# Kernel tuning notes

Measured on AMD Instinct MI355X. Metric: run time of the kernel, lower is better.

The kernel has to match this reference:

```python
import jax, jax.numpy as jnp
import numpy as np
from jax import lax


def setup_inputs() -> dict:
    key = jax.random.key(0)
    k1, k2 = jax.random.split(key)
    B, T, D, O = 8, 8192, 512, 512
    x = jax.random.normal(k1, (B, T, D), dtype=jnp.float32)
    # Dense kernel over concat([h_t, state]) -> width 2*D
    W = jax.random.normal(k2, (2 * D, O), dtype=jnp.float32) * (1.0 / np.sqrt(2 * D))
    b = jnp.zeros((O,), dtype=jnp.float32)
    decay = jnp.float32(0.95)
    return {"x": x, "W": W, "b": b, "decay": decay}


def reference(x, W, b, decay):
    # x: [B, T, D]; W: [2D, O]; b: [O]; decay: scalar lambda
    B, T, D = x.shape
    lam = jnp.clip(decay, 0.5, 0.999)  # keras constraint on the decay weight
    h_avg = jnp.mean(x, axis=0)  # [T, D] batch-mean per timestep

    # EMA recurrence: s_t = lam * s_{t-1} + (1 - lam) * h_avg_t, s_{-1} = 0
    def step(s, a):
        s = lam * s + (1.0 - lam) * a
        return s, s

    _, states = lax.scan(step, jnp.zeros((D,), x.dtype), h_avg)  # [T, D]

    # proj(concat([h_t, s_t])) = h_t @ W_h + s_t @ W_s + b (fused, no concat materialized)
    W_h, W_s = W[:D], W[D:]
    out = jnp.einsum('btd,do->bto', x, W_h) + jnp.einsum('td,do->to', states, W_s)[None] + b
    return out  # [B, T, O]
```

## Files before the change

kernel.cpp:

```cpp
#include <hip/hip_runtime.h>
#include <hip/hip_bf16.h>
#include <stdint.h>

#define T_DIM 8192
#define B_DIM 8
#define D_DIM 512
#define O_DIM 512

typedef __attribute__((ext_vector_type(4))) float f32x4;
typedef __attribute__((ext_vector_type(8))) short short8;
typedef __attribute__((ext_vector_type(4))) unsigned short us4;

__device__ __forceinline__ unsigned short f2bf(float f) {
  union { float f; uint32_t u; } v; v.f = f;
  uint32_t u = v.u + 0x7FFFu + ((v.u >> 16) & 1u);
  return (unsigned short)(u >> 16);
}

__device__ __forceinline__ uint32_t cvtpk(float a, float b) {
  uint32_t r;
  asm("v_cvt_pk_bf16_f32 %0, %1, %2" : "=v"(r) : "v"(a), "v"(b));
  return r;
}

__device__ __forceinline__ void gload_lds16(const void* g, void* l) {
  __builtin_amdgcn_global_load_lds(
      (const __attribute__((address_space(1))) void*)g,
      (__attribute__((address_space(3))) void*)l, 16, 0, 0);
}

__device__ __forceinline__ float clip_lam(const float* decay) {
  return fminf(fmaxf(decay[0], 0.5f), 0.999f);
}

__global__ void mean_kernel(const float* __restrict__ x, float* __restrict__ havg) {
  int idx = blockIdx.x * 256 + threadIdx.x;
  const f32x4* x4 = (const f32x4*)x;
  const size_t stride = (size_t)T_DIM * D_DIM / 4;
  f32x4 s = {0.f, 0.f, 0.f, 0.f};
#pragma unroll
  for (int b = 0; b < B_DIM; ++b) s += x4[(size_t)b * stride + idx];
  s *= 0.125f;
  ((f32x4*)havg)[idx] = s;
}

__global__ void wconv_kernel(const float* __restrict__ W, unsigned short* __restrict__ Wt) {
  __shared__ float tile[64][65];
  int bk = blockIdx.x >> 3;
  int bn = blockIdx.x & 7;
  int tr = threadIdx.x >> 4;
  int tc = threadIdx.x & 15;
#pragma unroll
  for (int i = 0; i < 4; ++i) {
    int row = i * 16 + tr;
    f32x4 v = *(const f32x4*)&W[(size_t)(bk * 64 + row) * O_DIM + bn * 64 + tc * 4];
#pragma unroll
    for (int j = 0; j < 4; ++j) tile[row][tc * 4 + j] = v[j];
  }
  __syncthreads();
#pragma unroll
  for (int i = 0; i < 4; ++i) {
    int nl = i * 16 + tr;
    us4 o;
#pragma unroll
    for (int j = 0; j < 4; ++j) o[j] = f2bf(tile[tc * 4 + j][nl]);
    int kg = bk * 64 + tc * 4;
    int h = kg >> 9;
    int k = kg & 511;
    *(us4*)&Wt[(size_t)h * (512 * 512) + (size_t)(bn * 64 + nl) * 512 + k] = o;
  }
}

#define CHUNK 128
#define NCHUNK (T_DIM / CHUNK)

__global__ void scanA_kernel(float* __restrict__ havg, const float* __restrict__ decay) {
  int chunk = blockIdx.x >> 1;
  int d = ((blockIdx.x & 1) << 8) + threadIdx.x;
  float lam = clip_lam(decay);
  float om = 1.0f - lam;
  size_t base = (size_t)chunk * CHUNK * D_DIM + d;
  float cur[16], nxt[16];
#pragma unroll
  for (int i = 0; i < 16; ++i) cur[i] = havg[base + (size_t)i * D_DIM];
  float s = 0.f;
  for (int blk = 0; blk < 8; ++blk) {
    if (blk < 7) {
#pragma unroll
      for (int i = 0; i < 16; ++i)
        nxt[i] = havg[base + (size_t)((blk + 1) * 16 + i) * D_DIM];
    }
#pragma unroll
    for (int i = 0; i < 16; ++i) {
      s = lam * s + om * cur[i];
      havg[base + (size_t)(blk * 16 + i) * D_DIM] = s;
    }
#pragma unroll
    for (int i = 0; i < 16; ++i) cur[i] = nxt[i];
  }
}

__global__ void scanB_kernel(const float* __restrict__ havg, const float* __restrict__ decay,
                             float* __restrict__ carry) {
  int d = blockIdx.x * 256 + threadIdx.x;
  float lam = clip_lam(decay);
  float l2 = lam * lam;
  float l4 = l2 * l2;
  float l8 = l4 * l4;
  float l16 = l8 * l8;
  float l32 = l16 * l16;
  float l64 = l32 * l32;
  float l128 = l64 * l64;
  float e[NCHUNK];
#pragma unroll
  for (int c = 0; c < NCHUNK; ++c)
    e[c] = havg[((size_t)c * CHUNK + CHUNK - 1) * D_DIM + d];
  float s = 0.f;
#pragma unroll
  for (int c = 0; c < NCHUNK; ++c) {
    s = l128 * s + e[c];
    carry[c * D_DIM + d] = s;
  }
}

__global__ void scanC_kernel(const float* __restrict__ havg, const float* __restrict__ carry,
                             const float* __restrict__ decay, unsigned short* __restrict__ st) {
  int idx = blockIdx.x * 256 + threadIdx.x;
  int t = idx >> 7;
  int d4 = idx & 127;
  int c = t >> 7;
  int k = t & 127;
  float lam = clip_lam(decay);
  float w = exp2f((float)(k + 1) * __log2f(lam));
  f32x4 p = ((const f32x4*)havg)[idx];
  f32x4 cin = {0.f, 0.f, 0.f, 0.f};
  if (c > 0) cin = ((const f32x4*)carry)[(size_t)(c - 1) * 128 + d4];
  us4 o;
#pragma unroll
  for (int j = 0; j < 4; ++j) o[j] = f2bf(p[j] + w * cin[j]);
  ((us4*)st)[idx] = o;
}

template <bool AF32, bool ADD_SBAR>
__global__ __launch_bounds__(256, 2)
void gemm128(const void* __restrict__ Av, const unsigned short* __restrict__ Bt,
             const float* __restrict__ extra, float* __restrict__ C) {
  constexpr int ABYTES = AF32 ? 16384 : 8192;
  __shared__ __align__(16) char smem[ABYTES + 8192];
  unsigned short* Bs = (unsigned short*)(smem + ABYTES);

  int nwg = gridDim.x;
  int bid = blockIdx.x;
  int swz = (bid & 7) * (nwg >> 3) + (bid >> 3);
  int tm = swz >> 2, tn = swz & 3;
  int brow = tm << 7, bcol = tn << 7;

  int tid = threadIdx.x;
  int wave = tid >> 6, lane = tid & 63;
  int wr = (wave >> 1) << 6, wc = (wave & 1) << 6;
  const int lr = lane & 15, lkb = lane >> 4;

  f32x4 acc[4][4];
#pragma unroll
  for (int m = 0; m < 4; ++m)
#pragma unroll
    for (int n = 0; n < 4; ++n) acc[m][n] = (f32x4){0.f, 0.f, 0.f, 0.f};

  for (int kt = 0; kt < 512 / 32; ++kt) {
    int k0 = kt << 5;
    if constexpr (AF32) {
      const float* Ag = (const float*)Av;
#pragma unroll
      for (int it = 0; it < 4; ++it) {
        int q = (it << 2) + wave;
        int row = (q << 3) + (lane >> 3);
        int kc = ((lane & 7) ^ (lane >> 3)) << 2;
        gload_lds16(Ag + (size_t)(brow + row) * 512 + k0 + kc, smem + (q << 10));
      }
    } else {
      const unsigned short* Ag = (const unsigned short*)Av;
#pragma unroll
      for (int it = 0; it < 2; ++it) {
        int q = (it << 2) + wave;
        int row = (q << 4) + (lane >> 2);
        int kc = (lane & 3) << 3;
        gload_lds16(Ag + (size_t)(brow + row) * 512 + k0 + kc, smem + (q << 10));
      }
    }
#pragma unroll
    for (int it = 0; it < 2; ++it) {
      int q = (it << 2) + wave;
      int n = (q << 4) + (lane >> 2);
      int kc = (lane & 3) << 3;
      gload_lds16(Bt + (size_t)(bcol + n) * 512 + k0 + kc, (char*)Bs + (q << 10));
    }
    __syncthreads();

    short8 af[4], bfr[4];
    if constexpr (AF32) {
      const float* As = (const float*)smem;
#pragma unroll
      for (int m = 0; m < 4; ++m) {
        int row = wr + (m << 4) + lr;
        int r7 = row & 7;
        int b0 = lkb << 1;
        f32x4 lo = *(const f32x4*)(As + row * 32 + ((b0 ^ r7) << 2));
        f32x4 hi = *(const f32x4*)(As + row * 32 + (((b0 + 1) ^ r7) << 2));
        union { short8 s; uint32_t u[4]; } t;
        t.u[0] = cvtpk(lo[0], lo[1]); t.u[1] = cvtpk(lo[2], lo[3]);
        t.u[2] = cvtpk(hi[0], hi[1]); t.u[3] = cvtpk(hi[2], hi[3]);
        af[m] = t.s;
      }
    } else {
      const unsigned short* As = (const unsigned short*)smem;
#pragma unroll
      for (int m = 0; m < 4; ++m)
        af[m] = *(const short8*)(As + (size_t)(wr + (m << 4) + lr) * 32 + (lkb << 3));
    }
#pragma unroll
    for (int n = 0; n < 4; ++n)
      bfr[n] = *(const short8*)(Bs + (size_t)(wc + (n << 4) + lr) * 32 + (lkb << 3));

#pragma unroll
    for (int m = 0; m < 4; ++m)
#pragma unroll
      for (int n = 0; n < 4; ++n)
        acc[m][n] = __builtin_amdgcn_mfma_f32_16x16x32_bf16(af[m], bfr[n], acc[m][n], 0, 0, 0);
    __syncthreads();
  }

#pragma unroll
  for (int m = 0; m < 4; ++m) {
    int row0 = brow + wr + (m << 4) + ((lane >> 4) << 2);
#pragma unroll
    for (int n = 0; n < 4; ++n) {
      int col = bcol + wc + (n << 4) + lr;
#pragma unroll
      for (int j = 0; j < 4; ++j) {
        int row = row0 + j;
        float v = acc[m][n][j];
        if constexpr (ADD_SBAR)
          v += extra[(size_t)(row & (T_DIM - 1)) * O_DIM + col];
        else
          v += extra[col];
        C[(size_t)row * O_DIM + col] = v;
      }
    }
  }
}

extern "C" void kernel_launch(void* const* d_in, const int* in_sizes, int n_in,
                              void* d_out, int out_size, void* d_ws, size_t ws_size,
                              hipStream_t stream) {
  (void)in_sizes; (void)n_in; (void)out_size; (void)ws_size;
  const float* x     = (const float*)d_in[0];
  const float* W     = (const float*)d_in[1];
  const float* bias  = (const float*)d_in[2];
  const float* decay = (const float*)d_in[3];
  float* out = (float*)d_out;

  char* ws = (char*)d_ws;
  float*          havg  = (float*)ws;
  unsigned short* st    = (unsigned short*)(ws + 16777216);
  unsigned short* Wt    = (unsigned short*)(ws + 16777216 + 8388608);
  float*          sbar  = (float*)(ws + 16777216 + 8388608 + 1048576);
  float*          carry = (float*)(ws + 16777216 + 8388608 + 1048576 + 16777216);

  mean_kernel<<<T_DIM * D_DIM / 4 / 256, 256, 0, stream>>>(x, havg);
  wconv_kernel<<<128, 256, 0, stream>>>(W, Wt);
  scanA_kernel<<<NCHUNK * 2, 256, 0, stream>>>(havg, decay);
  scanB_kernel<<<2, 256, 0, stream>>>(havg, decay, carry);
  scanC_kernel<<<T_DIM * D_DIM / 4 / 256, 256, 0, stream>>>(havg, carry, decay, st);
  gemm128<false, false><<<(T_DIM / 128) * 4, 256, 0, stream>>>(st, Wt + 512 * 512, bias, sbar);
  gemm128<true, true><<<(B_DIM * T_DIM / 128) * 4, 256, 0, stream>>>(x, Wt, sbar, out);
}
```

Measured before the change: 139.7 us.

## Double-buffer GEMM LDS tiles, swizzle bf16 LDS, vectorize epilogue via LDS

```diff
diff --git a/kernel.cpp b/kernel.cpp
--- a/kernel.cpp
+++ b/kernel.cpp
@@ -37,9 +37,10 @@
   int idx = blockIdx.x * 256 + threadIdx.x;
   const f32x4* x4 = (const f32x4*)x;
   const size_t stride = (size_t)T_DIM * D_DIM / 4;
-  f32x4 s = {0.f, 0.f, 0.f, 0.f};
-#pragma unroll
-  for (int b = 0; b < B_DIM; ++b) s += x4[(size_t)b * stride + idx];
+  f32x4 v[8];
+#pragma unroll
+  for (int b = 0; b < B_DIM; ++b) v[b] = x4[(size_t)b * stride + idx];
+  f32x4 s = ((v[0] + v[1]) + (v[2] + v[3])) + ((v[4] + v[5]) + (v[6] + v[7]));
   s *= 0.125f;
   ((f32x4*)havg)[idx] = s;
 }
@@ -142,12 +143,12 @@
 }
 
 template <bool AF32, bool ADD_SBAR>
-__global__ __launch_bounds__(256, 2)
+__global__ __launch_bounds__(256, AF32 ? 3 : 4)
 void gemm128(const void* __restrict__ Av, const unsigned short* __restrict__ Bt,
              const float* __restrict__ extra, float* __restrict__ C) {
   constexpr int ABYTES = AF32 ? 16384 : 8192;
-  __shared__ __align__(16) char smem[ABYTES + 8192];
-  unsigned short* Bs = (unsigned short*)(smem + ABYTES);
+  constexpr int BUFB = ABYTES + 8192;
+  __shared__ __align__(16) char smem[2][BUFB];
 
   int nwg = gridDim.x;
   int bid = blockIdx.x;
@@ -160,45 +161,63 @@
   int wr = (wave >> 1) << 6, wc = (wave & 1) << 6;
   const int lr = lane & 15, lkb = lane >> 4;
 
+  const int soct = ((lane & 3) ^ ((lane >> 3) & 3)) << 3;
+  const int pm = (lr >> 1) & 3;
+  const int kcA = ((lane & 7) ^ (lane >> 3)) << 2;
+
+  const size_t a_base = AF32
+      ? (size_t)(brow + (wave << 3) + (lane >> 3)) * 512 + kcA
+      : (size_t)(brow + (wave << 4) + (lane >> 2)) * 512 + soct;
+  const size_t b_base = (size_t)(bcol + (wave << 4) + (lane >> 2)) * 512 + soct;
+
   f32x4 acc[4][4];
 #pragma unroll
   for (int m = 0; m < 4; ++m)
 #pragma unroll
     for (int n = 0; n < 4; ++n) acc[m][n] = (f32x4){0.f, 0.f, 0.f, 0.f};
 
-  for (int kt = 0; kt < 512 / 32; ++kt) {
-    int k0 = kt << 5;
-    if constexpr (AF32) {
-      const float* Ag = (const float*)Av;
-#pragma unroll
-      for (int it = 0; it < 4; ++it) {
-        int q = (it << 2) + wave;
-        int row = (q << 3) + (lane >> 3);
-        int kc = ((lane & 7) ^ (lane >> 3)) << 2;
-        gload_lds16(Ag + (size_t)(brow + row) * 512 + k0 + kc, smem + (q << 10));
-      }
+#define STAGE(buf, kt_)                                                        \
+  {                                                                            \
+    int k0_ = (kt_) << 5;                                                      \
+    if constexpr (AF32) {                                                      \
+      const float* Ag = (const float*)Av;                                      \
+      _Pragma("unroll")                                                        \
+      for (int it = 0; it < 4; ++it)                                           \
+        gload_lds16(Ag + a_base + (size_t)(it << 14) + k0_,                    \
+                    &smem[buf][(((it << 2) + wave) << 10)]);                   \
+    } else {                                                                   \
+      const unsigned short* Ag = (const unsigned short*)Av;                    \
+      _Pragma("unroll")                                                        \
+      for (int it = 0; it < 2; ++it)                                           \
+        gload_lds16(Ag + a_base + (size_t)(it << 15) + k0_,                    \
+                    &smem[buf][(((it << 2) + wave) << 10)]);                   \
+    }                                                                          \
+    _Pragma("unroll")                                                          \
+    for (int it = 0; it < 2; ++it)                                             \
+      gload_lds16(Bt + b_base + (size_t)(it << 15) + k0_,                      \
+                  &smem[buf][ABYTES + (((it << 2) + wave) << 10)]);            \
+  }
+
+  STAGE(0, 0);
+
+#pragma unroll
+  for (int kt = 0; kt < 16; ++kt) {
+    const int cur = kt & 1;
+    if (kt < 15) {
+      STAGE(cur ^ 1, kt + 1);
+      if constexpr (AF32)
+        asm volatile("s_waitcnt vmcnt(6)" ::: "memory");
+      else
+        asm volatile("s_waitcnt vmcnt(4)" ::: "memory");
     } else {
-      const unsigned short* Ag = (const unsigned short*)Av;
-#pragma unroll
-      for (int it = 0; it < 2; ++it) {
-        int q = (it << 2) + wave;
-        int row = (q << 4) + (lane >> 2);
-        int kc = (lane & 3) << 3;
-        gload_lds16(Ag + (size_t)(brow + row) * 512 + k0 + kc, smem + (q << 10));
-      }
-    }
-#pragma unroll
-    for (int it = 0; it < 2; ++it) {
-      int q = (it << 2) + wave;
-      int n = (q << 4) + (lane >> 2);
-      int kc = (lane & 3) << 3;
-      gload_lds16(Bt + (size_t)(bcol + n) * 512 + k0 + kc, (char*)Bs + (q << 10));
-    }
-    __syncthreads();
+      asm volatile("s_waitcnt vmcnt(0)" ::: "memory");
+    }
+    __builtin_amdgcn_s_barrier();
+    __builtin_amdgcn_sched_barrier(0);
 
     short8 af[4], bfr[4];
     if constexpr (AF32) {
-      const float* As = (const float*)smem;
+      const float* As = (const float*)&smem[cur][0];
 #pragma unroll
       for (int m = 0; m < 4; ++m) {
         int row = wr + (m << 4) + lr;
@@ -212,40 +231,52 @@
         af[m] = t.s;
       }
     } else {
-      const unsigned short* As = (const unsigned short*)smem;
+      const unsigned short* As = (const unsigned short*)&smem[cur][0];
 #pragma unroll
       for (int m = 0; m < 4; ++m)
-        af[m] = *(const short8*)(As + (size_t)(wr + (m << 4) + lr) * 32 + (lkb << 3));
-    }
+        af[m] = *(const short8*)(As + (size_t)(wr + (m << 4) + lr) * 32 + ((lkb ^ pm) << 3));
+    }
+    const unsigned short* Bs = (const unsigned short*)&smem[cur][ABYTES];
 #pragma unroll
     for (int n = 0; n < 4; ++n)
-      bfr[n] = *(const short8*)(Bs + (size_t)(wc + (n << 4) + lr) * 32 + (lkb << 3));
+      bfr[n] = *(const short8*)(Bs + (size_t)(wc + (n << 4) + lr) * 32 + ((lkb ^ pm) << 3));
 
 #pragma unroll
     for (int m = 0; m < 4; ++m)
 #pragma unroll
       for (int n = 0; n < 4; ++n)
         acc[m][n] = __builtin_amdgcn_mfma_f32_16x16x32_bf16(af[m], bfr[n], acc[m][n], 0, 0, 0);
+
+    __builtin_amdgcn_sched_barrier(0);
+    __builtin_amdgcn_s_barrier();
+  }
+#undef STAGE
+
+  float* tp = (float*)&smem[0][0] + (size_t)wave * 2048;
+#pragma unroll
+  for (int m = 0; m < 4; ++m) {
+#pragma unroll
+    for (int n = 0; n < 4; ++n)
+#pragma unroll
+      for (int j = 0; j < 4; ++j)
+        tp[((lkb << 2) + j) * 68 + (n << 4) + lr] = acc[m][n][j];
     __syncthreads();
-  }
-
-#pragma unroll
-  for (int m = 0; m < 4; ++m) {
-    int row0 = brow + wr + (m << 4) + ((lane >> 4) << 2);
-#pragma unroll
-    for (int n = 0; n < 4; ++n) {
-      int col = bcol + wc + (n << 4) + lr;
-#pragma unroll
-      for (int j = 0; j < 4; ++j) {
-        int row = row0 + j;
-        float v = acc[m][n][j];
-        if constexpr (ADD_SBAR)
-          v += extra[(size_t)(row & (T_DIM - 1)) * O_DIM + col];
-        else
-          v += extra[col];
-        C[(size_t)row * O_DIM + col] = v;
-      }
-    }
+#pragma unroll
+    for (int p = 0; p < 4; ++p) {
+      int rl = (p << 2) + (lane >> 4);
+      int c0 = (lane & 15) << 2;
+      f32x4 v = *(const f32x4*)(tp + rl * 68 + c0);
+      int row = brow + wr + (m << 4) + rl;
+      int col = bcol + wc + c0;
+      f32x4 e;
+      if constexpr (ADD_SBAR)
+        e = *(const f32x4*)&extra[(size_t)(row & (T_DIM - 1)) * O_DIM + col];
+      else
+        e = *(const f32x4*)&extra[col];
+      v += e;
+      *(f32x4*)&C[(size_t)row * O_DIM + col] = v;
+    }
+    __syncthreads();
   }
 }
 
@@ -260,11 +291,12 @@
   float* out = (float*)d_out;
 
   char* ws = (char*)d_ws;
-  float*          havg  = (float*)ws;
-  unsigned short* st    = (unsigned short*)(ws + 16777216);
-  unsigned short* Wt    = (unsigned short*)(ws + 16777216 + 8388608);
-  float*          sbar  = (float*)(ws + 16777216 + 8388608 + 1048576);
-  float*          carry = (float*)(ws + 16777216 + 8388608 + 1048576 + 16777216);
+  size_t off = 0;
+  float*          havg  = (float*)(ws + off);          off += 16777216;
+  unsigned short* st    = (unsigned short*)(ws + off); off += 8388608;
+  unsigned short* Wt    = (unsigned short*)(ws + off); off += 1048576;
+  float*          sbar  = (float*)(ws + off);          off += 16777216;
+  float*          carry = (float*)(ws + off);          off += 131072;
 
   mean_kernel<<<T_DIM * D_DIM / 4 / 256, 256, 0, stream>>>(x, havg);
   wconv_kernel<<<128, 256, 0, stream>>>(W, Wt);
```

New measurement: 128.6 us. 1.09x faster.
